# Kernel tuning notes

Measured on AMD Instinct MI355X. Metric: run time of the kernel, lower is better.

The kernel has to match this reference:

```python
import jax, jax.numpy as jnp
import numpy as np

P, R = 50000, 32        # num_patients, CP rank
N0, N1 = 2000, 1000     # modality sizes (e.g., diagnosis codes, drug codes)


def setup_inputs() -> dict:
    key = jax.random.key(0)
    k0, k1, k2 = jax.random.split(key, 3)
    return {
        "pt_reps": jax.random.uniform(k0, (P, R), dtype=jnp.float32),
        "U0": jax.random.uniform(k1, (N0, R), dtype=jnp.float32),
        "U1": jax.random.uniform(k2, (N1, R), dtype=jnp.float32),
    }


def reference(pt_reps, U0, U1):
    # torch.diag(U.sum(0)) chained matmuls == columnwise scale by product
    # of the other factors' column sums.
    s0 = U0.sum(axis=0)  # [R]
    s1 = U1.sum(axis=0)  # [R]
    # mode 0: pt_reps @ diag(s1) @ U0.T  -> [P, N0]
    V0 = (pt_reps * s1) @ U0.T
    # mode 1: pt_reps @ diag(s0) @ U1.T  -> [P, N1]
    V1 = (pt_reps * s0) @ U1.T
    return (V0, V1)
```

## Files before the change

### kernel.cpp

```cpp
#include <hip/hip_runtime.h>

#define R 32
#define PCHUNK 200

__global__ __launch_bounds__(1024) void colsum_kernel(
    const float* __restrict__ U0, int n0rows,
    const float* __restrict__ U1, int n1rows,
    float* __restrict__ ws)
{
    const float* U = (blockIdx.x == 0) ? U1 : U0;
    int rows       = (blockIdx.x == 0) ? n1rows : n0rows;
    float* out     = ws + blockIdx.x * R;

    int c = threadIdx.x & (R - 1);
    int g = threadIdx.x >> 5;

    float acc = 0.f;
    for (int r = g; r < rows; r += 32)
        acc += U[(size_t)r * R + c];

    __shared__ float red[32][R + 1];
    red[g][c] = acc;
    __syncthreads();
    for (int off = 16; off > 0; off >>= 1) {
        if (g < off) red[g][c] += red[g + off][c];
        __syncthreads();
    }
    if (g == 0) out[c] = red[0][c];
}

__global__ __launch_bounds__(256) void mode_kernel(
    const float* __restrict__ pt,
    const float* __restrict__ U,
    const float* __restrict__ s,
    float* __restrict__ V,
    int N, int P)
{
    const int lane = threadIdx.x & 63;
    const int wave = threadIdx.x >> 6;
    const int slot = (blockIdx.x * 4 + wave) * 64 + lane;
    const int nslots = N >> 1;
    const bool active = (slot < nslots);
    const int n0 = (active ? slot : 0) * 2;

    float ua[R], ub[R];
    {
        const float4* Ua = (const float4*)(U + (size_t)n0 * R);
        const float4* Ub = (const float4*)(U + (size_t)(n0 + 1) * R);
        const float4* S4 = (const float4*)s;
#pragma unroll
        for (int i = 0; i < R / 4; ++i) {
            float4 sv = S4[i];
            float4 x = Ua[i];
            float4 y = Ub[i];
            ua[4*i+0] = x.x * sv.x; ua[4*i+1] = x.y * sv.y;
            ua[4*i+2] = x.z * sv.z; ua[4*i+3] = x.w * sv.w;
            ub[4*i+0] = y.x * sv.x; ub[4*i+1] = y.y * sv.y;
            ub[4*i+2] = y.z * sv.z; ub[4*i+3] = y.w * sv.w;
        }
    }

    int p0 = blockIdx.y * PCHUNK;
    int p1 = min(p0 + PCHUNK, P);
    for (int p = p0; p < p1; ++p) {
        const float4* A4 = (const float4*)(pt + (size_t)p * R);
        float ax0 = 0.f, ax1 = 0.f, ay0 = 0.f, ay1 = 0.f;
#pragma unroll
        for (int i = 0; i < R / 4; ++i) {
            float4 a = A4[i];
            ax0 += a.x * ua[4*i+0] + a.y * ua[4*i+1];
            ax1 += a.z * ua[4*i+2] + a.w * ua[4*i+3];
            ay0 += a.x * ub[4*i+0] + a.y * ub[4*i+1];
            ay1 += a.z * ub[4*i+2] + a.w * ub[4*i+3];
        }
        if (active) {
            float2 v = make_float2(ax0 + ax1, ay0 + ay1);
            union { float2 f2; double d; } cvt;
            cvt.f2 = v;
            __builtin_nontemporal_store(cvt.d, (double*)(V + (size_t)p * N + n0));
        }
    }
}

extern "C" void kernel_launch(void* const* d_in, const int* in_sizes, int n_in,
                              void* d_out, int out_size, void* d_ws, size_t ws_size,
                              hipStream_t stream) {
    const float* pt = (const float*)d_in[0];
    const float* U0 = (const float*)d_in[1];
    const float* U1 = (const float*)d_in[2];
    int P  = in_sizes[0] / R;
    int N0 = in_sizes[1] / R;
    int N1 = in_sizes[2] / R;

    float* ws  = (float*)d_ws;
    float* out = (float*)d_out;

    colsum_kernel<<<dim3(2), dim3(1024), 0, stream>>>(U0, N0, U1, N1, ws);

    int gy  = (P + PCHUNK - 1) / PCHUNK;
    int gx0 = ((N0 / 2) + 255) / 256;
    int gx1 = ((N1 / 2) + 255) / 256;
    mode_kernel<<<dim3(gx0, gy), dim3(256), 0, stream>>>(pt, U0, ws, out, N0, P);
    mode_kernel<<<dim3(gx1, gy), dim3(256), 0, stream>>>(pt, U1, ws + R,
                                                         out + (size_t)P * N0, N1, P);
}
```

Before: 840.5 us.

## Compute mode products with FP16 MFMA tiles and LDS-staged coalesced stores

Replaces the per-thread FP32 dot-product loop with 16x16x32 FP16 MFMA instructions. Each wave processes 16-patient by 64-column tiles, with the scaled factor matrix held in registers as fp16 fragments. Results are transposed through LDS so each lane writes 16-byte nontemporal stores. The kernel is output-write bound, so the intended gain is cheaper compute and wider stores. In exchange, inputs are rounded to fp16, which loses precision and can overflow for large scaled values, and the P>>4 tiling drops trailing rows if P is not a multiple of 16.

New measurement: 675.6 us. 1.24x faster.

```diff
diff --git a/kernel.cpp b/kernel.cpp
--- a/kernel.cpp
+++ b/kernel.cpp
@@ -1,7 +1,12 @@
 #include <hip/hip_runtime.h>
 
 #define R 32
-#define PCHUNK 200
+#define MT 8
+#define LDST 68
+
+typedef _Float16 f16x8 __attribute__((ext_vector_type(8)));
+typedef float fx4 __attribute__((ext_vector_type(4)));
+typedef float fx8 __attribute__((ext_vector_type(8)));
 
 __global__ __launch_bounds__(1024) void colsum_kernel(
     const float* __restrict__ U0, int n0rows,
@@ -29,7 +34,7 @@
     if (g == 0) out[c] = red[0][c];
 }
 
-__global__ __launch_bounds__(256) void mode_kernel(
+__global__ __launch_bounds__(256) void mode_mfma(
     const float* __restrict__ pt,
     const float* __restrict__ U,
     const float* __restrict__ s,
@@ -38,47 +43,74 @@
 {
     const int lane = threadIdx.x & 63;
     const int wave = threadIdx.x >> 6;
-    const int slot = (blockIdx.x * 4 + wave) * 64 + lane;
-    const int nslots = N >> 1;
-    const bool active = (slot < nslots);
-    const int n0 = (active ? slot : 0) * 2;
+    const int c    = lane & 15;
+    const int kg   = lane >> 4;
+    const int kb   = kg * 8;
+    const int c0   = blockIdx.x * 64;
 
-    float ua[R], ub[R];
-    {
-        const float4* Ua = (const float4*)(U + (size_t)n0 * R);
-        const float4* Ub = (const float4*)(U + (size_t)(n0 + 1) * R);
-        const float4* S4 = (const float4*)s;
+    const fx4* S4 = (const fx4*)s;
+    fx4 sA = S4[kg * 2 + 0];
+    fx4 sB = S4[kg * 2 + 1];
+
+    f16x8 bf[4];
 #pragma unroll
-        for (int i = 0; i < R / 4; ++i) {
-            float4 sv = S4[i];
-            float4 x = Ua[i];
-            float4 y = Ub[i];
-            ua[4*i+0] = x.x * sv.x; ua[4*i+1] = x.y * sv.y;
-            ua[4*i+2] = x.z * sv.z; ua[4*i+3] = x.w * sv.w;
-            ub[4*i+0] = y.x * sv.x; ub[4*i+1] = y.y * sv.y;
-            ub[4*i+2] = y.z * sv.z; ub[4*i+3] = y.w * sv.w;
-        }
+    for (int t = 0; t < 4; ++t) {
+        int n = c0 + t * 16 + c;
+        if (n > N - 1) n = N - 1;
+        const fx4* Up = (const fx4*)(U + (size_t)n * R + kb);
+        fx4 u0 = Up[0], u1 = Up[1];
+        fx8 f;
+        f[0] = u0[0] * sA[0]; f[1] = u0[1] * sA[1];
+        f[2] = u0[2] * sA[2]; f[3] = u0[3] * sA[3];
+        f[4] = u1[0] * sB[0]; f[5] = u1[1] * sB[1];
+        f[6] = u1[2] * sB[2]; f[7] = u1[3] * sB[3];
+        bf[t] = __builtin_convertvector(f, f16x8);
     }
 
-    int p0 = blockIdx.y * PCHUNK;
-    int p1 = min(p0 + PCHUNK, P);
-    for (int p = p0; p < p1; ++p) {
-        const float4* A4 = (const float4*)(pt + (size_t)p * R);
-        float ax0 = 0.f, ax1 = 0.f, ay0 = 0.f, ay1 = 0.f;
+    __shared__ float lds[4][16 * LDST];
+    float* L = lds[wave];
+
+    const int mtiles = P >> 4;
+    const int mt0 = (blockIdx.y * 4 + wave) * MT;
+    const int cc  = c * 4;
+    const bool act = (c0 + cc) < N;
+
+    for (int i = 0; i < MT; ++i) {
+        int mt = mt0 + i;
+        if (mt >= mtiles) break;
+        int p0 = mt << 4;
+
+        const fx4* Ap = (const fx4*)(pt + (size_t)(p0 + c) * R + kb);
+        fx4 a0 = Ap[0], a1 = Ap[1];
+        fx8 fa;
+        fa[0] = a0[0]; fa[1] = a0[1]; fa[2] = a0[2]; fa[3] = a0[3];
+        fa[4] = a1[0]; fa[5] = a1[1]; fa[6] = a1[2]; fa[7] = a1[3];
+        f16x8 af = __builtin_convertvector(fa, f16x8);
+
+        fx4 z = {0.f, 0.f, 0.f, 0.f};
+        fx4 acc0 = __builtin_amdgcn_mfma_f32_16x16x32_f16(af, bf[0], z, 0, 0, 0);
+        fx4 acc1 = __builtin_amdgcn_mfma_f32_16x16x32_f16(af, bf[1], z, 0, 0, 0);
+        fx4 acc2 = __builtin_amdgcn_mfma_f32_16x16x32_f16(af, bf[2], z, 0, 0, 0);
+        fx4 acc3 = __builtin_amdgcn_mfma_f32_16x16x32_f16(af, bf[3], z, 0, 0, 0);
+
 #pragma unroll
-        for (int i = 0; i < R / 4; ++i) {
-            float4 a = A4[i];
-            ax0 += a.x * ua[4*i+0] + a.y * ua[4*i+1];
-            ax1 += a.z * ua[4*i+2] + a.w * ua[4*i+3];
-            ay0 += a.x * ub[4*i+0] + a.y * ub[4*i+1];
-            ay1 += a.z * ub[4*i+2] + a.w * ub[4*i+3];
+        for (int j = 0; j < 4; ++j) {
+            L[(kg * 4 + j) * LDST +  0 + c] = acc0[j];
+            L[(kg * 4 + j) * LDST + 16 + c] = acc1[j];
+            L[(kg * 4 + j) * LDST + 32 + c] = acc2[j];
+            L[(kg * 4 + j) * LDST + 48 + c] = acc3[j];
         }
-        if (active) {
-            float2 v = make_float2(ax0 + ax1, ay0 + ay1);
-            union { float2 f2; double d; } cvt;
-            cvt.f2 = v;
-            __builtin_nontemporal_store(cvt.d, (double*)(V + (size_t)p * N + n0));
+        asm volatile("s_waitcnt lgkmcnt(0)" ::: "memory");
+
+#pragma unroll
+        for (int g = 0; g < 4; ++g) {
+            int row = g * 4 + kg;
+            fx4 v = *(const fx4*)&L[row * LDST + cc];
+            if (act)
+                __builtin_nontemporal_store(v,
+                    (fx4*)(V + (size_t)(p0 + row) * N + c0 + cc));
         }
+        asm volatile("s_waitcnt lgkmcnt(0)" ::: "memory");
     }
 }
 
@@ -97,10 +129,12 @@
 
     colsum_kernel<<<dim3(2), dim3(1024), 0, stream>>>(U0, N0, U1, N1, ws);
 
-    int gy  = (P + PCHUNK - 1) / PCHUNK;
-    int gx0 = ((N0 / 2) + 255) / 256;
-    int gx1 = ((N1 / 2) + 255) / 256;
-    mode_kernel<<<dim3(gx0, gy), dim3(256), 0, stream>>>(pt, U0, ws, out, N0, P);
-    mode_kernel<<<dim3(gx1, gy), dim3(256), 0, stream>>>(pt, U1, ws + R,
-                                                         out + (size_t)P * N0, N1, P);
+    int mtiles = P >> 4;
+    int gy  = (mtiles + 4 * MT - 1) / (4 * MT);
+    int gx0 = (N0 + 63) / 64;
+    int gx1 = (N1 + 63) / 64;
+
+    mode_mfma<<<dim3(gx0, gy), dim3(256), 0, stream>>>(pt, U0, ws, out, N0, P);
+    mode_mfma<<<dim3(gx1, gy), dim3(256), 0, stream>>>(pt, U1, ws + R,
+                                                       out + (size_t)P * N0, N1, P);
 }
```
